# Kernel optimization log

Hardware: AMD Instinct MI355X
Metric: run time of the kernel (lower is better)

## Reference

```python
import jax, jax.numpy as jnp
import numpy as np

NUM_HEADS = 16
HEAD_DIM = 128
ROTARY_DIM = 32  # head_dim * rotary_pct(0.25)
ROPE_BASE = 10000.0
SCALE = HEAD_DIM ** -0.5


def _rotate_half(x):
    x1, x2 = jnp.split(x, 2, axis=-1)
    return jnp.concatenate((-x2, x1), axis=-1)


def _rope_tables(seq_len, dtype):
    inv_freq = 1.0 / (ROPE_BASE ** (jnp.arange(0, ROTARY_DIM, 2, dtype=jnp.float32) / ROTARY_DIM))
    freqs = jnp.arange(seq_len, dtype=jnp.float32)[:, None] * inv_freq[None, :]  # [S, rd/2]
    emb = jnp.concatenate((freqs, freqs), axis=-1)  # [S, rd]
    return jnp.cos(emb).astype(dtype), jnp.sin(emb).astype(dtype)


def setup_inputs() -> dict:
    key = jax.random.key(0)
    k1, k2, k3 = jax.random.split(key, 3)
    B, S, H = 2, 2048, 2048
    hidden_states = jax.random.normal(k1, (B, S, H), dtype=jnp.float32)
    attention_mask = jnp.zeros((B, 1, S, S), dtype=jnp.float32)
    Wqkv = jax.random.normal(k2, (H, 3 * H), dtype=jnp.float32) * (H ** -0.5)
    Wout = jax.random.normal(k3, (H, H), dtype=jnp.float32) * (H ** -0.5)
    return {"hidden_states": hidden_states, "attention_mask": attention_mask,
            "Wqkv": Wqkv, "Wout": Wout}


def reference(hidden_states, attention_mask, Wqkv, Wout):
    B, S, H = hidden_states.shape
    qkv = jnp.einsum('bsh,hk->bsk', hidden_states, Wqkv)  # [B,S,3H]
    q, k, v = jnp.split(qkv, 3, axis=-1)

    def to_heads(x):
        return x.reshape(B, S, NUM_HEADS, HEAD_DIM).transpose(0, 2, 1, 3)  # [B,nh,S,hd]

    q, k, v = to_heads(q), to_heads(k), to_heads(v)

    cos, sin = _rope_tables(S, hidden_states.dtype)  # [S, ROTARY_DIM]
    cos = cos[None, None, :, :]
    sin = sin[None, None, :, :]

    def rope(x):
        xr = x[..., :ROTARY_DIM]
        xr = xr * cos + _rotate_half(xr) * sin
        return jnp.concatenate((xr, x[..., ROTARY_DIM:]), axis=-1)

    q, k = rope(q), rope(k)

    scores = jnp.einsum('bhqd,bhkd->bhqk', q, k) * SCALE + attention_mask
    probs = jax.nn.softmax(scores, axis=-1)  # dropout p=0 -> identity
    ctx = jnp.einsum('bhqk,bhkd->bhqd', probs, v)
    ctx = ctx.transpose(0, 2, 1, 3).reshape(B, S, H)
    return jnp.einsum('bsh,ho->bso', ctx, Wout)
```

## Files before the change

kernel.cpp:

```cpp
#include <hip/hip_runtime.h>

typedef __attribute__((ext_vector_type(4))) float f32x4;
typedef __attribute__((ext_vector_type(16))) float f32x16;
typedef __attribute__((ext_vector_type(8))) short s16x8;
typedef __attribute__((ext_vector_type(4))) unsigned short u16x4;
typedef __attribute__((ext_vector_type(8))) unsigned short u16x8;

#define DEVINL __device__ __forceinline__

constexpr int Bb = 2;
constexpr int Ss = 2048;
constexpr int Hh = 2048;
constexpr int NH = 16;
constexpr int HD = 128;
constexpr float ATT_SCALE = 0.08838834764831845f;
constexpr float CEXP = ATT_SCALE * 1.44269504089f;
constexpr float INV_SCALE = 11.313708498984761f;
constexpr float RAW_THR = 90.50966799f;

DEVINL unsigned short f2bf(float f) {
    unsigned u = __float_as_uint(f);
    u += 0x7FFFu + ((u >> 16) & 1u);
    return (unsigned short)(u >> 16);
}
DEVINL float bf2f(unsigned short h) { return __uint_as_float(((unsigned)h) << 16); }
DEVINL float fexp2(float x) { return __builtin_amdgcn_exp2f(x); }

DEVINL void gl16(const void* g, void* l) {
    __builtin_amdgcn_global_load_lds((const __attribute__((address_space(1))) void*)g,
                                     (__attribute__((address_space(3))) void*)l, 16, 0, 0);
}

__global__ void scan_mask_k(const float* __restrict__ m, int* __restrict__ flag) {
    size_t i = ((size_t)blockIdx.x * 256 + threadIdx.x) * 4;
    f32x4 v = *(const f32x4*)(m + i);
    int any = (v[0] != 0.f) || (v[1] != 0.f) || (v[2] != 0.f) || (v[3] != 0.f);
    if (__any(any)) { if ((threadIdx.x & 63) == 0) atomicOr(flag, 1); }
}

__global__ void convH_k(const float* __restrict__ x, unsigned short* __restrict__ y) {
    size_t i = (size_t)blockIdx.x * 256 + threadIdx.x;
    f32x4 a = *(const f32x4*)(x + i * 8);
    f32x4 b = *(const f32x4*)(x + i * 8 + 4);
    u16x8 o;
    o[0] = f2bf(a[0]); o[1] = f2bf(a[1]); o[2] = f2bf(a[2]); o[3] = f2bf(a[3]);
    o[4] = f2bf(b[0]); o[5] = f2bf(b[1]); o[6] = f2bf(b[2]); o[7] = f2bf(b[3]);
    *(u16x8*)(y + i * 8) = o;
}

__global__ void convT_k(const float* __restrict__ W, unsigned short* __restrict__ Wt,
                        int R, int C) {
    __shared__ float tile[32][33];
    int c0 = blockIdx.x * 32, r0 = blockIdx.y * 32;
    int t = threadIdx.x;
    int rr = t >> 3, cc = (t & 7) * 4;
    f32x4 v = *(const f32x4*)(W + (size_t)(r0 + rr) * C + c0 + cc);
    tile[rr][cc + 0] = v[0]; tile[rr][cc + 1] = v[1];
    tile[rr][cc + 2] = v[2]; tile[rr][cc + 3] = v[3];
    __syncthreads();
    u16x4 o;
    o[0] = f2bf(tile[cc + 0][rr]); o[1] = f2bf(tile[cc + 1][rr]);
    o[2] = f2bf(tile[cc + 2][rr]); o[3] = f2bf(tile[cc + 3][rr]);
    *(u16x4*)(Wt + (size_t)(c0 + rr) * R + r0 + cc) = o;
}

template<int MODE>
__global__ __launch_bounds__(512, 2)
void gemm128x256_k(const unsigned short* __restrict__ A, const unsigned short* __restrict__ Bt,
                   float* __restrict__ Cf, unsigned short* __restrict__ Cb,
                   unsigned short* __restrict__ VtOut,
                   int M, int N, int K, int rm, int rn, int snx) {
    __shared__ char lds[98304];
    int t = threadIdx.x, w = t >> 6, ln = t & 63, lr = ln & 15, lg = ln >> 4;
    int wm = w >> 2, wn = w & 3;
    int f = blockIdx.x;
    int xcd = f & 7, i0 = f >> 3;
    int mb = (xcd / snx) * rm + i0 % rm;
    int nb = (xcd % snx) * rn + i0 / rm;
    int m0 = mb * 128, n0 = nb * 256;
    const char* Ab = (const char*)A;
    const char* Bbp = (const char*)Bt;

    f32x4 acc[4][4];
#pragma unroll
    for (int i = 0; i < 4; ++i)
#pragma unroll
        for (int j = 0; j < 4; ++j) { acc[i][j][0] = 0.f; acc[i][j][1] = 0.f; acc[i][j][2] = 0.f; acc[i][j][3] = 0.f; }

    auto STGA = [&](int sbuf, int skh, int kt) {
        int row = t >> 2, c = t & 3;
        int cs = c ^ ((row >> 1) & 3);
        gl16(Ab + ((size_t)(m0 + row) * K + kt * 64 + skh * 32) * 2 + cs * 16,
             lds + sbuf * 49152 + skh * 8192 + t * 16);
    };
    auto STGB = [&](int sbuf, int skh, int kt) {
#pragma unroll
        for (int rr = 0; rr < 2; ++rr) {
            int ci = rr * 512 + t;
            int row = ci >> 2, c = ci & 3;
            int cs = c ^ ((row >> 1) & 3);
            gl16(Bbp + ((size_t)(n0 + row) * K + kt * 64 + skh * 32) * 2 + cs * 16,
                 lds + sbuf * 49152 + 16384 + skh * 16384 + ci * 16);
        }
    };

#define PH128(buf, kh, sbuf, skh, st)                                             \
  {                                                                               \
    const char* Ap = lds + (buf) * 49152 + (kh) * 8192;                           \
    const char* Bp = lds + (buf) * 49152 + 16384 + (kh) * 16384;                  \
    s16x8 af[4], bfr[4];                                                          \
    _Pragma("unroll")                                                             \
    for (int i = 0; i < 4; ++i) {                                                 \
      int row = wm * 64 + i * 16 + lr;                                            \
      af[i] = *(const s16x8*)(Ap + row * 64 + ((lg ^ ((row >> 1) & 3)) * 16));    \
    }                                                                             \
    _Pragma("unroll")                                                             \
    for (int j = 0; j < 4; ++j) {                                                 \
      int row = wn * 64 + j * 16 + lr;                                            \
      bfr[j] = *(const s16x8*)(Bp + row * 64 + ((lg ^ ((row >> 1) & 3)) * 16));   \
    }                                                                             \
    STGA(sbuf, skh, st); STGB(sbuf, skh, st);                                     \
    __builtin_amdgcn_s_barrier();                                                 \
    asm volatile("s_waitcnt lgkmcnt(0)" ::: "memory");                            \
    __builtin_amdgcn_s_setprio(1);                                                \
    _Pragma("unroll")                                                             \
    for (int i = 0; i < 4; ++i)                                                   \
      _Pragma("unroll")                                                           \
      for (int j = 0; j < 4; ++j)                                                 \
        acc[i][j] = __builtin_amdgcn_mfma_f32_16x16x32_bf16(af[i], bfr[j],        \
                                                            acc[i][j], 0, 0, 0); \
    __builtin_amdgcn_s_setprio(0);                                                \
    asm volatile("s_waitcnt vmcnt(6)" ::: "memory");                              \
    __builtin_amdgcn_s_barrier();                                                 \
  }

    const int NT = K >> 6;
    STGA(0, 0, 0); STGB(0, 0, 0);
    STGA(0, 1, 0); STGB(0, 1, 0);
    STGA(1, 0, 1); STGB(1, 0, 1);
    asm volatile("s_waitcnt vmcnt(3)" ::: "memory");
    __builtin_amdgcn_s_barrier();

    for (int it = 0; it < (NT >> 1); ++it) {
        int e = it * 2;
        int e2 = (e + 2 < NT) ? e + 2 : e;
        int e3 = (e + 3 < NT) ? e + 3 : e + 1;
        PH128(0, 0,  1, 1, e + 1)
        PH128(0, 1,  0, 0, e2)
        PH128(1, 0,  0, 1, e2)
        PH128(1, 1,  1, 0, e3)
    }
    asm volatile("s_waitcnt vmcnt(0)" ::: "memory");
#undef PH128

    if (MODE == 0 && n0 >= 4096) {
#pragma unroll
        for (int i = 0; i < 4; ++i)
#pragma unroll
            for (int j = 0; j < 4; ++j) {
                int vcol = n0 - 4096 + wn * 64 + j * 16 + lr;
                int h = vcol >> 7, d = vcol & 127;
                int gr = m0 + wm * 64 + i * 16 + lg * 4;
                int bb = gr >> 11, si = gr & 2047;
                u16x4 o;
                o[0] = f2bf(acc[i][j][0]); o[1] = f2bf(acc[i][j][1]);
                o[2] = f2bf(acc[i][j][2]); o[3] = f2bf(acc[i][j][3]);
                *(u16x4*)(VtOut + ((size_t)(bb * 16 + h) * 128 + d) * 2048 + si) = o;
            }
        return;
    }

    if (MODE == 0 && (wn & 1) == 0) {
        float invf = fexp2((float)lr * -0.83048202372f);
#pragma unroll
        for (int i = 0; i < 4; ++i)
#pragma unroll
            for (int r = 0; r < 4; ++r) {
                int srow = (m0 + wm * 64 + i * 16 + lg * 4 + r) & (Ss - 1);
                float sn, cs;
                sincosf((float)srow * invf, &sn, &cs);
                float x1 = acc[i][0][r], x2 = acc[i][1][r];
                acc[i][0][r] = x1 * cs - x2 * sn;
                acc[i][1][r] = x2 * cs + x1 * sn;
            }
    }

#pragma unroll
    for (int i = 0; i < 4; ++i)
#pragma unroll
        for (int j = 0; j < 4; ++j)
#pragma unroll
            for (int r = 0; r < 4; ++r) {
                int gr = m0 + wm * 64 + i * 16 + lg * 4 + r;
                int gc = n0 + wn * 64 + j * 16 + lr;
                float vv = acc[i][j][r];
                if (MODE == 1) Cf[(size_t)gr * N + gc] = vv;
                else           Cb[(size_t)gr * N + gc] = f2bf(vv);
            }
}

__global__ __launch_bounds__(512)
void attn_k(const unsigned short* __restrict__ qkv, const unsigned short* __restrict__ Vt,
            const float* __restrict__ mask, unsigned short* __restrict__ ctxb,
            const int* __restrict__ flag) {
    __shared__ char ldsK[2][16384];
    __shared__ char ldsV[2][16384];
    int f = blockIdx.x;
    int swzb = (f & 7) * 32 + (f >> 3);
    int bh = swzb >> 3, qt = swzb & 7;
    int b = bh >> 4, h = bh & 15;
    int t = threadIdx.x, w = t >> 6, ln = t & 63;
    int q5 = ln & 31, lg5 = ln >> 5;
    int useMask = *flag;
    int qb = qt * 256 + w * 32;
    const char* qkvB = (const char*)qkv;
    const char* VtB = (const char*)Vt;

    auto STAGE = [&](int buf, int kk0s) {
#pragma unroll
        for (int c = 0; c < 2; ++c) {
            int ci = c * 512 + t;
            int krow = ci >> 4, kcb = (ci & 15) << 4;
            gl16(qkvB + (((size_t)(b * Ss + kk0s + krow)) * 6144 + 2048 + h * 128) * 2 + (kcb ^ ((krow & 15) << 4)),
                 ldsK[buf] + ci * 16);
            int vrow = ci >> 3, vcb = (ci & 7) << 4;
            gl16(VtB + (((size_t)(bh * 128 + vrow)) * 2048 + kk0s) * 2 + (vcb ^ ((vrow & 7) << 4)),
                 ldsV[buf] + ci * 16);
        }
    };

    s16x8 qf[8];
    size_t qrow = ((size_t)(b * Ss + qb + q5)) * 6144 + h * 128;
#pragma unroll
    for (int dc = 0; dc < 8; ++dc) qf[dc] = *(const s16x8*)(qkv + qrow + dc * 16 + lg5 * 8);

    float mr = -3e38f, lsum = 0.f;
    f32x16 ctx[4];
#pragma unroll
    for (int dt = 0; dt < 4; ++dt)
#pragma unroll
        for (int r = 0; r < 16; ++r) ctx[dt][r] = 0.f;
    const float* mrow = mask + (size_t)b * Ss * Ss;

    STAGE(0, 0);
    asm volatile("s_waitcnt vmcnt(0)" ::: "memory");
    __builtin_amdgcn_s_barrier();

    for (int tix = 0; tix < 32; ++tix) {
        int kk0 = tix * 64;
        int cur = tix & 1;
        if (kk0 + 64 < Ss) STAGE(cur ^ 1, kk0 + 64);

        f32x16 st[2];
#pragma unroll
        for (int n = 0; n < 2; ++n) {
            f32x16 sacc;
#pragma unroll
            for (int r = 0; r < 16; ++r) sacc[r] = 0.f;
            int krow = n * 32 + q5;
            const char* kb = ldsK[cur] + krow * 256;
            int sw = krow & 15;
            __builtin_amdgcn_s_setprio(1);
#pragma unroll
            for (int dc = 0; dc < 8; ++dc) {
                s16x8 kf = *(const s16x8*)(kb + (((dc * 2 + lg5) ^ sw) << 4));
                sacc = __builtin_amdgcn_mfma_f32_32x32x16_bf16(kf, qf[dc], sacc, 0, 0, 0);
            }
            __builtin_amdgcn_s_setprio(0);
            st[n] = sacc;
        }
        if (useMask) {
#pragma unroll
            for (int n = 0; n < 2; ++n)
#pragma unroll
                for (int r = 0; r < 16; ++r) {
                    int kk = n * 32 + (r & 3) + 8 * (r >> 2) + 4 * lg5;
                    st[n][r] += mrow[(size_t)(qb + q5) * Ss + kk0 + kk] * INV_SCALE;
                }
        }
        float pmax = st[0][0];
#pragma unroll
        for (int n = 0; n < 2; ++n)
#pragma unroll
            for (int r = 0; r < 16; ++r) pmax = fmaxf(pmax, st[n][r]);
        pmax = fmaxf(pmax, __shfl_xor(pmax, 32));
        bool need = pmax > mr + RAW_THR;
        if (__any(need)) {
            float mn = fmaxf(mr, pmax);
            float al = fexp2((mr - mn) * CEXP);
            mr = mn;
            lsum *= al;
#pragma unroll
            for (int dt = 0; dt < 4; ++dt)
#pragma unroll
                for (int r = 0; r < 16; ++r)
                    ctx[dt][r] *= __shfl(al, (r & 3) + 8 * (r >> 2) + 4 * lg5);
        }
        float mC = mr * CEXP;
        float rs = 0.f;
#pragma unroll
        for (int n = 0; n < 2; ++n)
#pragma unroll
            for (int r = 0; r < 16; ++r) {
                float p = fexp2(st[n][r] * CEXP - mC);
                rs += p;
                st[n][r] = p;
            }
        rs += __shfl_xor(rs, 32);
        lsum += rs;
        s16x8 paf[4];
#pragma unroll
        for (int c = 0; c < 4; ++c) {
            const f32x16 sv = st[c >> 1];
            const int cc = (c & 1) * 8;
            unsigned loA = (unsigned)f2bf(sv[cc + 0]) | ((unsigned)f2bf(sv[cc + 1]) << 16);
            unsigned loB = (unsigned)f2bf(sv[cc + 2]) | ((unsigned)f2bf(sv[cc + 3]) << 16);
            unsigned hiA = (unsigned)f2bf(sv[cc + 4]) | ((unsigned)f2bf(sv[cc + 5]) << 16);
            unsigned hiB = (unsigned)f2bf(sv[cc + 6]) | ((unsigned)f2bf(sv[cc + 7]) << 16);
            unsigned sendA = lg5 ? loA : hiA;
            unsigned sendB = lg5 ? loB : hiB;
            unsigned recvA = (unsigned)__shfl_xor((int)sendA, 32);
            unsigned recvB = (unsigned)__shfl_xor((int)sendB, 32);
            union { s16x8 v; unsigned u[4]; } pu;
            pu.u[0] = lg5 ? recvA : loA;
            pu.u[1] = lg5 ? recvB : loB;
            pu.u[2] = lg5 ? hiA : recvA;
            pu.u[3] = lg5 ? hiB : recvB;
            paf[c] = pu.v;
        }
#pragma unroll
        for (int dt = 0; dt < 4; ++dt) {
            int vrow = dt * 32 + q5;
            const char* vb = ldsV[cur] + vrow * 128;
            int swv = vrow & 7;
            __builtin_amdgcn_s_setprio(1);
#pragma unroll
            for (int c = 0; c < 4; ++c) {
                s16x8 vf = *(const s16x8*)(vb + (((c * 2 + lg5) ^ swv) << 4));
                ctx[dt] = __builtin_amdgcn_mfma_f32_32x32x16_bf16(paf[c], vf, ctx[dt], 0, 0, 0);
            }
            __builtin_amdgcn_s_setprio(0);
        }
        asm volatile("s_waitcnt vmcnt(0)" ::: "memory");
        __builtin_amdgcn_s_barrier();
    }
#pragma unroll
    for (int r = 0; r < 16; ++r) {
        int qr = (r & 3) + 8 * (r >> 2) + 4 * lg5;
        float li = 1.f / __shfl(lsum, qr);
        size_t base = ((size_t)(b * Ss + qb + qr)) * Hh + h * 128 + q5;
#pragma unroll
        for (int dt = 0; dt < 4; ++dt)
            ctxb[base + dt * 32] = f2bf(ctx[dt][r] * li);
    }
}

extern "C" void kernel_launch(void* const* d_in, const int* in_sizes, int n_in,
                              void* d_out, int out_size, void* d_ws, size_t ws_size,
                              hipStream_t stream) {
    (void)in_sizes; (void)n_in; (void)out_size; (void)ws_size;
    const float* hidden = (const float*)d_in[0];
    const float* mask   = (const float*)d_in[1];
    const float* Wqkv   = (const float*)d_in[2];
    const float* Wout   = (const float*)d_in[3];
    float* out = (float*)d_out;

    char* ws = (char*)d_ws;
    size_t off = 0;
    auto alloc = [&](size_t bytes) { char* p = ws + off; off += (bytes + 255) & ~(size_t)255; return p; };
    unsigned short* hbf   = (unsigned short*)alloc((size_t)8388608 * 2);
    unsigned short* wqkvT = (unsigned short*)alloc((size_t)12582912 * 2);
    unsigned short* woutT = (unsigned short*)alloc((size_t)4194304 * 2);
    unsigned short* qkv   = (unsigned short*)alloc((size_t)25165824 * 2);
    unsigned short* Vt    = (unsigned short*)alloc((size_t)8388608 * 2);
    int* flag             = (int*)alloc(256);
    unsigned short* ctx = hbf;

    hipMemsetAsync(flag, 0, 4, stream);
    scan_mask_k<<<8192, 256, 0, stream>>>(mask, flag);
    convH_k<<<4096, 256, 0, stream>>>(hidden, hbf);
    convT_k<<<dim3(192, 64), 256, 0, stream>>>(Wqkv, wqkvT, 2048, 6144);
    convT_k<<<dim3(64, 64), 256, 0, stream>>>(Wout, woutT, 2048, 2048);
    gemm128x256_k<0><<<768, 512, 0, stream>>>(hbf, wqkvT, nullptr, qkv, Vt,
                                              4096, 6144, 2048, 16, 6, 4);
    attn_k<<<256, 512, 0, stream>>>(qkv, Vt, mask, ctx, flag);
    gemm128x256_k<1><<<256, 512, 0, stream>>>(ctx, woutT, out, nullptr, nullptr,
                                              4096, 2048, 2048, 16, 2, 4);
}
```

Before: 297.5 us.

## Replace 128x256 GEMM with simpler 128x128 double-buffered GEMM kernel

Rewrites the projection GEMM as a 128x128 tile kernel with 256 threads (4 waves in a 2x2 arrangement), a 64-wide K step with two LDS buffers and a new XOR swizzle. The half-tile ping-pong pipeline with split barriers is replaced by a plain prefetch-next, compute-current loop. Grid sizes double for both GEMMs. The aim is more blocks and better occupancy and load balance. The cost is lower arithmetic reuse per tile and a full vmcnt(0) wait plus barrier every K step, which reduces overlap of loads with compute.

```diff
diff --git a/kernel.cpp b/kernel.cpp
--- a/kernel.cpp
+++ b/kernel.cpp
@@ -65,19 +65,19 @@
 }
 
 template<int MODE>
-__global__ __launch_bounds__(512, 2)
-void gemm128x256_k(const unsigned short* __restrict__ A, const unsigned short* __restrict__ Bt,
-                   float* __restrict__ Cf, unsigned short* __restrict__ Cb,
-                   unsigned short* __restrict__ VtOut,
-                   int M, int N, int K, int rm, int rn, int snx) {
-    __shared__ char lds[98304];
+__global__ __launch_bounds__(256, 2)
+void gemm128_k(const unsigned short* __restrict__ A, const unsigned short* __restrict__ Bt,
+               float* __restrict__ Cf, unsigned short* __restrict__ Cb,
+               unsigned short* __restrict__ VtOut,
+               int M, int N, int K, int rm, int rn, int snx) {
+    __shared__ char lds[65536];
     int t = threadIdx.x, w = t >> 6, ln = t & 63, lr = ln & 15, lg = ln >> 4;
-    int wm = w >> 2, wn = w & 3;
+    int wr = w >> 1, wc = w & 1;
     int f = blockIdx.x;
     int xcd = f & 7, i0 = f >> 3;
     int mb = (xcd / snx) * rm + i0 % rm;
     int nb = (xcd % snx) * rn + i0 / rm;
-    int m0 = mb * 128, n0 = nb * 256;
+    int m0 = mb * 128, n0 = nb * 128;
     const char* Ab = (const char*)A;
     const char* Bbp = (const char*)Bt;
 
@@ -87,80 +87,60 @@
 #pragma unroll
         for (int j = 0; j < 4; ++j) { acc[i][j][0] = 0.f; acc[i][j][1] = 0.f; acc[i][j][2] = 0.f; acc[i][j][3] = 0.f; }
 
-    auto STGA = [&](int sbuf, int skh, int kt) {
-        int row = t >> 2, c = t & 3;
-        int cs = c ^ ((row >> 1) & 3);
-        gl16(Ab + ((size_t)(m0 + row) * K + kt * 64 + skh * 32) * 2 + cs * 16,
-             lds + sbuf * 49152 + skh * 8192 + t * 16);
+    auto STAGE = [&](int buf, int kt) {
+        char* dA = lds + buf * 32768;
+        char* dB = dA + 16384;
+        size_t kb = ((size_t)kt * 64) * 2;
+#pragma unroll
+        for (int ld = 0; ld < 4; ++ld) {
+            int ci = ld * 256 + t;
+            int row = ci >> 3, cb = (ci & 7) << 4;
+            int sc = cb ^ ((row & 7) << 4);
+            gl16(Ab + ((size_t)(m0 + row) * K) * 2 + kb + sc, dA + ci * 16);
+            gl16(Bbp + ((size_t)(n0 + row) * K) * 2 + kb + sc, dB + ci * 16);
+        }
     };
-    auto STGB = [&](int sbuf, int skh, int kt) {
-#pragma unroll
-        for (int rr = 0; rr < 2; ++rr) {
-            int ci = rr * 512 + t;
-            int row = ci >> 2, c = ci & 3;
-            int cs = c ^ ((row >> 1) & 3);
-            gl16(Bbp + ((size_t)(n0 + row) * K + kt * 64 + skh * 32) * 2 + cs * 16,
-                 lds + sbuf * 49152 + 16384 + skh * 16384 + ci * 16);
-        }
-    };
-
-#define PH128(buf, kh, sbuf, skh, st)                                             \
-  {                                                                               \
-    const char* Ap = lds + (buf) * 49152 + (kh) * 8192;                           \
-    const char* Bp = lds + (buf) * 49152 + 16384 + (kh) * 16384;                  \
-    s16x8 af[4], bfr[4];                                                          \
-    _Pragma("unroll")                                                             \
-    for (int i = 0; i < 4; ++i) {                                                 \
-      int row = wm * 64 + i * 16 + lr;                                            \
-      af[i] = *(const s16x8*)(Ap + row * 64 + ((lg ^ ((row >> 1) & 3)) * 16));    \
-    }                                                                             \
-    _Pragma("unroll")                                                             \
-    for (int j = 0; j < 4; ++j) {                                                 \
-      int row = wn * 64 + j * 16 + lr;                                            \
-      bfr[j] = *(const s16x8*)(Bp + row * 64 + ((lg ^ ((row >> 1) & 3)) * 16));   \
-    }                                                                             \
-    STGA(sbuf, skh, st); STGB(sbuf, skh, st);                                     \
-    __builtin_amdgcn_s_barrier();                                                 \
-    asm volatile("s_waitcnt lgkmcnt(0)" ::: "memory");                            \
-    __builtin_amdgcn_s_setprio(1);                                                \
-    _Pragma("unroll")                                                             \
-    for (int i = 0; i < 4; ++i)                                                   \
-      _Pragma("unroll")                                                           \
-      for (int j = 0; j < 4; ++j)                                                 \
-        acc[i][j] = __builtin_amdgcn_mfma_f32_16x16x32_bf16(af[i], bfr[j],        \
-                                                            acc[i][j], 0, 0, 0); \
-    __builtin_amdgcn_s_setprio(0);                                                \
-    asm volatile("s_waitcnt vmcnt(6)" ::: "memory");                              \
-    __builtin_amdgcn_s_barrier();                                                 \
-  }
 
     const int NT = K >> 6;
-    STGA(0, 0, 0); STGB(0, 0, 0);
-    STGA(0, 1, 0); STGB(0, 1, 0);
-    STGA(1, 0, 1); STGB(1, 0, 1);
-    asm volatile("s_waitcnt vmcnt(3)" ::: "memory");
+    STAGE(0, 0);
+    asm volatile("s_waitcnt vmcnt(0)" ::: "memory");
     __builtin_amdgcn_s_barrier();
 
-    for (int it = 0; it < (NT >> 1); ++it) {
-        int e = it * 2;
-        int e2 = (e + 2 < NT) ? e + 2 : e;
-        int e3 = (e + 3 < NT) ? e + 3 : e + 1;
-        PH128(0, 0,  1, 1, e + 1)
-        PH128(0, 1,  0, 0, e2)
-        PH128(1, 0,  0, 1, e2)
-        PH128(1, 1,  1, 0, e3)
-    }
-    asm volatile("s_waitcnt vmcnt(0)" ::: "memory");
-#undef PH128
+    for (int kt = 0; kt < NT; ++kt) {
+        int cur = kt & 1;
+        if (kt + 1 < NT) STAGE(cur ^ 1, kt + 1);
+        const char* As = lds + cur * 32768;
+        const char* Bs = As + 16384;
+#pragma unroll
+        for (int kc = 0; kc < 2; ++kc) {
+            s16x8 af[4], bfr[4];
+#pragma unroll
+            for (int i = 0; i < 4; ++i) {
+                int rowa = wr * 64 + i * 16 + lr;
+                af[i] = *(const s16x8*)(As + rowa * 128 + ((kc * 64 + lg * 16) ^ ((rowa & 7) << 4)));
+                int rowb = wc * 64 + i * 16 + lr;
+                bfr[i] = *(const s16x8*)(Bs + rowb * 128 + ((kc * 64 + lg * 16) ^ ((rowb & 7) << 4)));
+            }
+            __builtin_amdgcn_s_setprio(1);
+#pragma unroll
+            for (int i = 0; i < 4; ++i)
+#pragma unroll
+                for (int j = 0; j < 4; ++j)
+                    acc[i][j] = __builtin_amdgcn_mfma_f32_16x16x32_bf16(af[i], bfr[j], acc[i][j], 0, 0, 0);
+            __builtin_amdgcn_s_setprio(0);
+        }
+        asm volatile("s_waitcnt vmcnt(0)" ::: "memory");
+        __builtin_amdgcn_s_barrier();
+    }
 
     if (MODE == 0 && n0 >= 4096) {
 #pragma unroll
         for (int i = 0; i < 4; ++i)
 #pragma unroll
             for (int j = 0; j < 4; ++j) {
-                int vcol = n0 - 4096 + wn * 64 + j * 16 + lr;
+                int vcol = n0 - 4096 + wc * 64 + j * 16 + lr;
                 int h = vcol >> 7, d = vcol & 127;
-                int gr = m0 + wm * 64 + i * 16 + lg * 4;
+                int gr = m0 + wr * 64 + i * 16 + lg * 4;
                 int bb = gr >> 11, si = gr & 2047;
                 u16x4 o;
                 o[0] = f2bf(acc[i][j][0]); o[1] = f2bf(acc[i][j][1]);
@@ -170,13 +150,13 @@
         return;
     }
 
-    if (MODE == 0 && (wn & 1) == 0) {
+    if (MODE == 0 && wc == 0) {
         float invf = fexp2((float)lr * -0.83048202372f);
 #pragma unroll
         for (int i = 0; i < 4; ++i)
 #pragma unroll
             for (int r = 0; r < 4; ++r) {
-                int srow = (m0 + wm * 64 + i * 16 + lg * 4 + r) & (Ss - 1);
+                int srow = (m0 + wr * 64 + i * 16 + lg * 4 + r) & (Ss - 1);
                 float sn, cs;
                 sincosf((float)srow * invf, &sn, &cs);
                 float x1 = acc[i][0][r], x2 = acc[i][1][r];
@@ -191,8 +171,8 @@
         for (int j = 0; j < 4; ++j)
 #pragma unroll
             for (int r = 0; r < 4; ++r) {
-                int gr = m0 + wm * 64 + i * 16 + lg * 4 + r;
-                int gc = n0 + wn * 64 + j * 16 + lr;
+                int gr = m0 + wr * 64 + i * 16 + lg * 4 + r;
+                int gc = n0 + wc * 64 + j * 16 + lr;
                 float vv = acc[i][j][r];
                 if (MODE == 1) Cf[(size_t)gr * N + gc] = vv;
                 else           Cb[(size_t)gr * N + gc] = f2bf(vv);
@@ -381,9 +361,9 @@
     convH_k<<<4096, 256, 0, stream>>>(hidden, hbf);
     convT_k<<<dim3(192, 64), 256, 0, stream>>>(Wqkv, wqkvT, 2048, 6144);
     convT_k<<<dim3(64, 64), 256, 0, stream>>>(Wout, woutT, 2048, 2048);
-    gemm128x256_k<0><<<768, 512, 0, stream>>>(hbf, wqkvT, nullptr, qkv, Vt,
-                                              4096, 6144, 2048, 16, 6, 4);
+    gemm128_k<0><<<1536, 256, 0, stream>>>(hbf, wqkvT, nullptr, qkv, Vt,
+                                           4096, 6144, 2048, 16, 12, 4);
     attn_k<<<256, 512, 0, stream>>>(qkv, Vt, mask, ctx, flag);
-    gemm128x256_k<1><<<256, 512, 0, stream>>>(ctx, woutT, out, nullptr, nullptr,
-                                              4096, 2048, 2048, 16, 2, 4);
-}
+    gemm128_k<1><<<512, 256, 0, stream>>>(ctx, woutT, out, nullptr, nullptr,
+                                          4096, 2048, 2048, 16, 4, 4);
+}
```

After: 290.5 us, median of 3. 2.3% less time.
